# Kernel tuning notes

Measured on AMD Instinct MI355X. Metric: run time of the kernel, lower is better.

The kernel has to match this reference:

```python
import jax, jax.numpy as jnp
import numpy as np

B, N, C = 4, 20480, 128
H, HD = 8, 16           # num_heads, head_dim (C // H)
L = 4                   # number of WindowBasedGraphAttentionBlocks
NW, WS = 320, 64        # num_windows, window_size (N // NW)
SCALE = HD ** -0.5
EPS = 1e-5


def layernorm(x, g, b):
    mu = jnp.mean(x, axis=-1, keepdims=True)
    var = jnp.mean(jnp.square(x - mu), axis=-1, keepdims=True)
    return (x - mu) * jax.lax.rsqrt(var + EPS) * g + b


def setup_inputs() -> dict:
    key = jax.random.key(0)
    ks = jax.random.split(key, 8)
    x = jax.random.normal(ks[0], (B, N, C), dtype=jnp.float32)
    # geodesic window mapping: each of NW windows has exactly WS members, permuted
    window_ids = jnp.asarray(
        np.random.RandomState(0).permutation(np.repeat(np.arange(NW), WS)),
        dtype=jnp.int32)
    s = 0.02
    inp = {
        'x': x,
        'g1': jnp.ones((L, C), jnp.float32),
        'be1': jnp.zeros((L, C), jnp.float32),
        'Wqkv': jax.random.normal(ks[1], (L, C, 3 * C), jnp.float32) * s,
        'bqkv': jnp.zeros((L, 3 * C), jnp.float32),
        'rel_bias': jax.random.normal(ks[2], (L, H, 1, 1), jnp.float32) * s,
        'Wproj': jax.random.normal(ks[3], (L, C, C), jnp.float32) * s,
        'bproj': jnp.zeros((L, C), jnp.float32),
        'g2': jnp.ones((L, C), jnp.float32),
        'be2': jnp.zeros((L, C), jnp.float32),
        'W1': jax.random.normal(ks[4], (L, C, 4 * C), jnp.float32) * s,
        'b1': jnp.zeros((L, 4 * C), jnp.float32),
        'W2': jax.random.normal(ks[5], (L, 4 * C, C), jnp.float32) * s,
        'b2': jnp.zeros((L, C), jnp.float32),
        'window_ids': window_ids,
    }
    return inp


def _encoder(x, g1, be1, Wqkv, bqkv, rel_bias, Wproj, bproj, g2, be2,
             W1, b1, W2, b2, sort_idx, inv_idx):
    def step(x, p):
        (g1, be1, Wqkv, bqkv, rb, Wp, bp, g2, be2, W1, b1, W2, b2) = p
        shortcut = x
        # GeodesicWindowPartition: gather by argsort(window_ids), split into windows
        win = x[:, sort_idx, :].reshape(B * NW, WS, C)
        h = layernorm(win, g1, be1)
        qkv = (h @ Wqkv + bqkv).reshape(B * NW, WS, 3, H, HD)
        q = qkv[:, :, 0].transpose(0, 2, 1, 3)  # [BW, H, WS, HD]
        k = qkv[:, :, 1].transpose(0, 2, 1, 3)
        v = qkv[:, :, 2].transpose(0, 2, 1, 3)
        attn = jnp.einsum('whqd,whkd->whqk', q, k) * SCALE
        attn = attn + rb[None]                  # relative geometry bias [H,1,1]
        attn = jax.nn.softmax(attn, axis=-1)
        out = jnp.einsum('whqk,whkd->whqd', attn, v)
        out = out.transpose(0, 2, 1, 3).reshape(B * NW, WS, C)
        out = out @ Wp + bp                     # AttentionOutputProjection
        rec = out.reshape(B, N, C)[:, inv_idx, :]  # partition.reverse
        x = shortcut + rec
        h2 = layernorm(x, g2, be2)
        x = x + (jax.nn.gelu(h2 @ W1 + b1) @ W2 + b2)
        return x, None

    params = (g1, be1, Wqkv, bqkv, rel_bias, Wproj, bproj, g2, be2, W1, b1, W2, b2)
    x, _ = jax.lax.scan(step, x, params)
    return x


def reference(x, g1, be1, Wqkv, bqkv, rel_bias, Wproj, bproj, g2, be2,
              W1, b1, W2, b2, window_ids):
    sort_idx = jnp.argsort(window_ids)
    inv_idx = jnp.argsort(sort_idx)
    return _encoder(x, g1, be1, Wqkv, bqkv, rel_bias, Wproj, bproj, g2, be2,
                    W1, b1, W2, b2, sort_idx, inv_idx)
```

## Files before the change

### kernel.cpp

```cpp
#include <hip/hip_runtime.h>
#include <hip/hip_bf16.h>
#include <math.h>

#define Nn 20480
#define Cc 128
#define Hh 8
#define Ll 4
#define NWw 320
#define BN 81920

typedef short sv8 __attribute__((ext_vector_type(8)));
typedef __bf16 bfv8 __attribute__((ext_vector_type(8)));
typedef float f32x4 __attribute__((ext_vector_type(4)));

__device__ __forceinline__ f32x4 mfma16(sv8 a, sv8 b, f32x4 c) {
    return __builtin_amdgcn_mfma_f32_16x16x32_bf16(
        __builtin_bit_cast(bfv8, a), __builtin_bit_cast(bfv8, b), c, 0, 0, 0);
}
__device__ __forceinline__ ushort f2bf(float f) {
    uint u = __float_as_uint(f);
    u += 0x7fffu + ((u >> 16) & 1u);
    return (ushort)(u >> 16);
}
__device__ __forceinline__ uint pk2bf(float lo, float hi) {
    uint r;
    asm("v_cvt_pk_bf16_f32 %0, %1, %2" : "=v"(r) : "v"(lo), "v"(hi));
    return r;
}
__device__ __forceinline__ float fast_gelu(float x) {
    float z = 0.7978845608f * (x + 0.044715f * x * x * x);
    return x * __builtin_amdgcn_rcpf(1.0f + __expf(-2.0f * z));
}

__global__ __launch_bounds__(64) void rank_kernel(const int* __restrict__ wid,
        int* __restrict__ lrank, int* __restrict__ hist) {
    __shared__ int keys[64];
    int c = blockIdx.x, lane = threadIdx.x;
    for (int j = lane; j < NWw; j += 64) hist[c * NWw + j] = 0;
    int i = c * 64 + lane;
    int w = wid[i];
    keys[lane] = w;
    __syncthreads();
    int rank = 0, total = 0;
    for (int j = 0; j < 64; ++j) {
        int kj = keys[j];
        total += (kj == w);
        rank += (j < lane && kj == w) ? 1 : 0;
    }
    lrank[i] = rank;
    if (rank == 0) hist[c * NWw + w] = total;
}
__global__ __launch_bounds__(64) void prefix_kernel(int* __restrict__ hist) {
    int w = blockIdx.x, lane = threadIdx.x;
    int running = 0;
    for (int it = 0; it < NWw / 64; ++it) {
        int c = it * 64 + lane;
        int v = hist[c * NWw + w];
        int orig = v;
        #pragma unroll
        for (int d = 1; d < 64; d <<= 1) {
            int tt = __shfl_up(v, d, 64);
            if (lane >= d) v += tt;
        }
        hist[c * NWw + w] = running + v - orig;
        running += __shfl(v, 63, 64);
    }
}
__global__ __launch_bounds__(64) void scatter_kernel(const int* __restrict__ wid,
        const int* __restrict__ lrank, const int* __restrict__ hist,
        int* __restrict__ sidx) {
    int c = blockIdx.x, lane = threadIdx.x;
    int i = c * 64 + lane;
    int w = wid[i];
    sidx[w * 64 + hist[c * NWw + w] + lrank[i]] = i;
}

__global__ __launch_bounds__(256) void wconv_kernel(
    const float* __restrict__ Wqkv, const float* __restrict__ Wproj,
    const float* __restrict__ W1, const float* __restrict__ W2,
    ushort* __restrict__ wt) {
    int id = blockIdx.x * 256 + threadIdx.x;
    int l = id / 196608;
    int r = id % 196608;
    const float* src; int dst;
    if (r < 49152) { int n = r % 384, k = r / 384;
        src = Wqkv + l * 49152 + k * 384 + n; dst = l * 196608 + n * 128 + k; }
    else if (r < 65536) { int rr = r - 49152; int n = rr % 128, k = rr / 128;
        src = Wproj + l * 16384 + k * 128 + n; dst = l * 196608 + 49152 + n * 128 + k; }
    else if (r < 131072) { int rr = r - 65536; int n = rr % 512, k = rr / 512;
        src = W1 + l * 65536 + k * 512 + n; dst = l * 196608 + 65536 + n * 128 + k; }
    else { int rr = r - 131072; int n = rr % 128, k = rr / 128;
        src = W2 + l * 65536 + k * 128 + n; dst = l * 196608 + 131072 + n * 512 + k; }
    wt[dst] = f2bf(*src);
}

__global__ __launch_bounds__(256, 2) void attn_fused_kernel(
    const float* __restrict__ xsrc, float* __restrict__ xdst,
    const ushort* __restrict__ wqkvT, const float* __restrict__ bqkv,
    const float* __restrict__ relb, const ushort* __restrict__ wprojT,
    const float* __restrict__ bproj, const float* __restrict__ g1,
    const float* __restrict__ be1, const int* __restrict__ sidx) {
    __shared__ __align__(16) ushort hl_[64][128];
    __shared__ __align__(16) ushort qkn[64][256];
    __shared__ __align__(16) ushort vT[128][76];
    __shared__ __align__(16) ushort pt[4][16][76];
    __shared__ int ridx[64];

    int t = threadIdx.x;
    int wave = t >> 6, lane = t & 63;
    int lr = lane & 15, lg = lane >> 4;
    int wb = blockIdx.x;
    int bN = (wb / NWw) * Nn;
    int p0 = (wb % NWw) * 64;

    if (t < 64) ridx[t] = sidx[p0 + t];
    __syncthreads();

    {
        int hl2 = lane & 31, hb = lane >> 5;
        float4 gg = *(const float4*)(g1 + hl2 * 4);
        float4 bb = *(const float4*)(be1 + hl2 * 4);
        #pragma unroll
        for (int it = 0; it < 8; ++it) {
            int row = it * 8 + wave * 2 + hb;
            int gi = bN + ridx[row];
            float4 v = *(const float4*)(xsrc + (size_t)gi * Cc + hl2 * 4);
            float s = v.x + v.y + v.z + v.w;
            s += __shfl_xor(s, 1, 64);  s += __shfl_xor(s, 2, 64);
            s += __shfl_xor(s, 4, 64);  s += __shfl_xor(s, 8, 64);
            s += __shfl_xor(s, 16, 64);
            float mu = s * 0.0078125f;
            float d0 = v.x - mu, d1 = v.y - mu, d2 = v.z - mu, d3 = v.w - mu;
            float q = d0 * d0 + d1 * d1 + d2 * d2 + d3 * d3;
            q += __shfl_xor(q, 1, 64);  q += __shfl_xor(q, 2, 64);
            q += __shfl_xor(q, 4, 64);  q += __shfl_xor(q, 8, 64);
            q += __shfl_xor(q, 16, 64);
            float rs = rsqrtf(q * 0.0078125f + 1e-5f);
            uint2 pk;
            pk.x = pk2bf(d0 * rs * gg.x + bb.x, d1 * rs * gg.y + bb.y);
            pk.y = pk2bf(d2 * rs * gg.z + bb.z, d3 * rs * gg.w + bb.w);
            *(uint2*)&hl_[row][(hl2 * 4) ^ ((row & 7) << 3)] = pk;
        }
    }
    __syncthreads();

    {
        f32x4 acc[4][6] = {};
        #pragma unroll
        for (int ks = 0; ks < 4; ++ks) {
            int k0 = ks * 32 + lg * 8;
            sv8 a[4], b[6];
            #pragma unroll
            for (int rf = 0; rf < 4; ++rf) {
                int row = rf * 16 + lr;
                a[rf] = *(const sv8*)&hl_[row][k0 ^ ((row & 7) << 3)];
            }
            #pragma unroll
            for (int nf = 0; nf < 6; ++nf) {
                int gcol = (nf < 2 ? 32 * wave + nf * 16
                          : nf < 4 ? 128 + 32 * wave + (nf - 2) * 16
                                   : 256 + 32 * wave + (nf - 4) * 16) + lr;
                b[nf] = *(const sv8*)(wqkvT + (size_t)gcol * 128 + k0);
            }
            #pragma unroll
            for (int rf = 0; rf < 4; ++rf)
                #pragma unroll
                for (int nf = 0; nf < 6; ++nf)
                    acc[rf][nf] = mfma16(a[rf], b[nf], acc[rf][nf]);
        }
        #pragma unroll
        for (int nf = 0; nf < 6; ++nf) {
            int gcol = (nf < 2 ? 32 * wave + nf * 16
                      : nf < 4 ? 128 + 32 * wave + (nf - 2) * 16
                               : 256 + 32 * wave + (nf - 4) * 16) + lr;
            float bs = bqkv[gcol];
            if (nf < 4) {
                #pragma unroll
                for (int rf = 0; rf < 4; ++rf)
                    #pragma unroll
                    for (int r = 0; r < 4; ++r) {
                        int row = rf * 16 + lg * 4 + r;
                        qkn[row][gcol ^ ((row & 7) << 3)] = f2bf(acc[rf][nf][r] + bs);
                    }
            } else {
                int dcol = gcol - 256;
                #pragma unroll
                for (int rf = 0; rf < 4; ++rf) {
                    uint2 pk;
                    pk.x = pk2bf(acc[rf][nf][0] + bs, acc[rf][nf][1] + bs);
                    pk.y = pk2bf(acc[rf][nf][2] + bs, acc[rf][nf][3] + bs);
                    *(uint2*)&vT[dcol][rf * 16 + lg * 4] = pk;
                }
            }
        }
    }
    __syncthreads();

    f32x4 zz = {0.f, 0.f, 0.f, 0.f};
    #pragma unroll
    for (int hi = 0; hi < 2; ++hi) {
        int hh = wave * 2 + hi;
        float rb = relb[hh];
        sv8 bv[2];
        #pragma unroll
        for (int ks = 0; ks < 2; ++ks)
            bv[ks] = *(const sv8*)&vT[hh * 16 + lr][ks * 32 + lg * 8];
        sv8 aq[4], bk[4];
        sv8 z = {0, 0, 0, 0, 0, 0, 0, 0};
        bool lo = (lg < 2);
        #pragma unroll
        for (int f = 0; f < 4; ++f) {
            aq[f] = z; bk[f] = z;
            if (lo) {
                int row = f * 16 + lr;
                aq[f] = *(const sv8*)&qkn[row][(hh * 16 + lg * 8) ^ ((row & 7) << 3)];
                bk[f] = *(const sv8*)&qkn[row][(128 + hh * 16 + lg * 8) ^ ((row & 7) << 3)];
            }
        }
        f32x4 s[4][4];
        #pragma unroll
        for (int kt = 0; kt < 4; ++kt)
            #pragma unroll
            for (int qt = 0; qt < 4; ++qt)
                s[kt][qt] = mfma16(bk[kt], aq[qt], zz);

        f32x4 o[4];
        #pragma unroll
        for (int qt = 0; qt < 4; ++qt) {
            float v[16];
            #pragma unroll
            for (int kt = 0; kt < 4; ++kt)
                #pragma unroll
                for (int r = 0; r < 4; ++r)
                    v[kt * 4 + r] = s[kt][qt][r] * 0.25f + rb;
            float m0 = fmaxf(fmaxf(fmaxf(v[0], v[1]), fmaxf(v[2], v[3])),
                             fmaxf(fmaxf(v[4], v[5]), fmaxf(v[6], v[7])));
            float m1 = fmaxf(fmaxf(fmaxf(v[8], v[9]), fmaxf(v[10], v[11])),
                             fmaxf(fmaxf(v[12], v[13]), fmaxf(v[14], v[15])));
            float mx = fmaxf(m0, m1);
            mx = fmaxf(mx, __shfl_xor(mx, 16, 64));
            mx = fmaxf(mx, __shfl_xor(mx, 32, 64));
            float sum = 0.f;
            #pragma unroll
            for (int i = 0; i < 16; ++i) {
                v[i] = __expf(v[i] - mx);
                sum += v[i];
            }
            sum += __shfl_xor(sum, 16, 64);
            sum += __shfl_xor(sum, 32, 64);
            float inv = __builtin_amdgcn_rcpf(sum);
            #pragma unroll
            for (int kt = 0; kt < 4; ++kt) {
                uint2 pk;
                pk.x = pk2bf(v[kt * 4 + 0] * inv, v[kt * 4 + 1] * inv);
                pk.y = pk2bf(v[kt * 4 + 2] * inv, v[kt * 4 + 3] * inv);
                *(uint2*)&pt[wave][lr][kt * 16 + lg * 4] = pk;
            }
            sv8 ap0 = *(const sv8*)&pt[wave][lr][lg * 8];
            sv8 ap1 = *(const sv8*)&pt[wave][lr][32 + lg * 8];
            o[qt] = mfma16(ap0, bv[0], zz);
            o[qt] = mfma16(ap1, bv[1], o[qt]);
        }
        #pragma unroll
        for (int qt = 0; qt < 4; ++qt)
            #pragma unroll
            for (int r = 0; r < 4; ++r) {
                int row = qt * 16 + lg * 4 + r;
                hl_[row][(hh * 16 + lr) ^ ((row & 7) << 3)] = f2bf(o[qt][r]);
            }
    }
    __syncthreads();

    {
        f32x4 acc[4][2] = {};
        #pragma unroll
        for (int ks = 0; ks < 4; ++ks) {
            int k0 = ks * 32 + lg * 8;
            sv8 a[4], b[2];
            #pragma unroll
            for (int rf = 0; rf < 4; ++rf) {
                int row = rf * 16 + lr;
                a[rf] = *(const sv8*)&hl_[row][k0 ^ ((row & 7) << 3)];
            }
            #pragma unroll
            for (int nf = 0; nf < 2; ++nf)
                b[nf] = *(const sv8*)(wprojT + (size_t)(wave * 32 + nf * 16 + lr) * 128 + k0);
            #pragma unroll
            for (int rf = 0; rf < 4; ++rf)
                #pragma unroll
                for (int nf = 0; nf < 2; ++nf)
                    acc[rf][nf] = mfma16(a[rf], b[nf], acc[rf][nf]);
        }
        #pragma unroll
        for (int nf = 0; nf < 2; ++nf) {
            int col = wave * 32 + nf * 16 + lr;
            float bs = bproj[col];
            #pragma unroll
            for (int rf = 0; rf < 4; ++rf)
                #pragma unroll
                for (int r = 0; r < 4; ++r) {
                    int row = rf * 16 + lg * 4 + r;
                    int gi = bN + ridx[row];
                    size_t ad = (size_t)gi * Cc + col;
                    xdst[ad] = xsrc[ad] + acc[rf][nf][r] + bs;
                }
        }
    }
}

__global__ __launch_bounds__(256, 3) void mlp_fused_kernel(
    const float* __restrict__ xsrc, float* __restrict__ xdst,
    const ushort* __restrict__ w1T, const float* __restrict__ b1,
    const ushort* __restrict__ w2T, const float* __restrict__ b2,
    const float* __restrict__ g2, const float* __restrict__ be2) {
    __shared__ __align__(16) char smem[49152];
    ushort (*hl_)[128] = (ushort (*)[128])smem;
    ushort (*hid)[64][128] = (ushort (*)[64][128])(smem + 16384);
    int t = threadIdx.x, wave = t >> 6, lane = t & 63;
    int lr = lane & 15, lg = lane >> 4;
    int r0 = blockIdx.x * 64;

    {
        int hl2 = lane & 31, hb = lane >> 5;
        float4 gg = *(const float4*)(g2 + hl2 * 4);
        float4 bb = *(const float4*)(be2 + hl2 * 4);
        #pragma unroll
        for (int it = 0; it < 8; ++it) {
            int row = it * 8 + wave * 2 + hb;
            float4 v = *(const float4*)(xsrc + (size_t)(r0 + row) * Cc + hl2 * 4);
            float s = v.x + v.y + v.z + v.w;
            s += __shfl_xor(s, 1, 64);  s += __shfl_xor(s, 2, 64);
            s += __shfl_xor(s, 4, 64);  s += __shfl_xor(s, 8, 64);
            s += __shfl_xor(s, 16, 64);
            float mu = s * 0.0078125f;
            float d0 = v.x - mu, d1 = v.y - mu, d2 = v.z - mu, d3 = v.w - mu;
            float q = d0 * d0 + d1 * d1 + d2 * d2 + d3 * d3;
            q += __shfl_xor(q, 1, 64);  q += __shfl_xor(q, 2, 64);
            q += __shfl_xor(q, 4, 64);  q += __shfl_xor(q, 8, 64);
            q += __shfl_xor(q, 16, 64);
            float rs = rsqrtf(q * 0.0078125f + 1e-5f);
            uint2 pk;
            pk.x = pk2bf(d0 * rs * gg.x + bb.x, d1 * rs * gg.y + bb.y);
            pk.y = pk2bf(d2 * rs * gg.z + bb.z, d3 * rs * gg.w + bb.w);
            *(uint2*)&hl_[row][(hl2 * 4) ^ ((row & 7) << 3)] = pk;
        }
    }
    __syncthreads();

    f32x4 acc2[4][2] = {};
    #pragma unroll
    for (int c = 0; c < 4; ++c) {
        int cb = c & 1;
        f32x4 acc[4][2] = {};
        #pragma unroll
        for (int ks = 0; ks < 4; ++ks) {
            int k0 = ks * 32 + lg * 8;
            sv8 a[4], b[2];
            #pragma unroll
            for (int rf = 0; rf < 4; ++rf) {
                int row = rf * 16 + lr;
                a[rf] = *(const sv8*)&hl_[row][k0 ^ ((row & 7) << 3)];
            }
            #pragma unroll
            for (int nf = 0; nf < 2; ++nf)
                b[nf] = *(const sv8*)(w1T + (size_t)(c * 128 + wave * 32 + nf * 16 + lr) * 128 + k0);
            #pragma unroll
            for (int rf = 0; rf < 4; ++rf)
                #pragma unroll
                for (int nf = 0; nf < 2; ++nf)
                    acc[rf][nf] = mfma16(a[rf], b[nf], acc[rf][nf]);
        }
        #pragma unroll
        for (int nf = 0; nf < 2; ++nf) {
            int lcol = wave * 32 + nf * 16 + lr;
            float bs = b1[c * 128 + lcol];
            #pragma unroll
            for (int rf = 0; rf < 4; ++rf)
                #pragma unroll
                for (int r = 0; r < 4; ++r) {
                    int row = rf * 16 + lg * 4 + r;
                    hid[cb][row][lcol ^ ((row & 7) << 3)] = f2bf(fast_gelu(acc[rf][nf][r] + bs));
                }
        }
        __syncthreads();
        #pragma unroll
        for (int ks = 0; ks < 4; ++ks) {
            int k0 = ks * 32 + lg * 8;
            sv8 a[4], b[2];
            #pragma unroll
            for (int rf = 0; rf < 4; ++rf) {
                int row = rf * 16 + lr;
                a[rf] = *(const sv8*)&hid[cb][row][k0 ^ ((row & 7) << 3)];
            }
            #pragma unroll
            for (int nf = 0; nf < 2; ++nf)
                b[nf] = *(const sv8*)(w2T + (size_t)(wave * 32 + nf * 16 + lr) * 512 + c * 128 + k0);
            #pragma unroll
            for (int rf = 0; rf < 4; ++rf)
                #pragma unroll
                for (int nf = 0; nf < 2; ++nf)
                    acc2[rf][nf] = mfma16(a[rf], b[nf], acc2[rf][nf]);
        }
    }
    __syncthreads();

    {
        float* fh = (float*)smem;
        #pragma unroll
        for (int nf = 0; nf < 2; ++nf) {
            int col = wave * 32 + nf * 16 + lr;
            float bs = b2[col];
            #pragma unroll
            for (int rf = 0; rf < 4; ++rf)
                #pragma unroll
                for (int r = 0; r < 4; ++r) {
                    int row = rf * 16 + lg * 4 + r;
                    fh[row * 132 + col] = acc2[rf][nf][r] + bs;
                }
        }
        __syncthreads();
        #pragma unroll
        for (int j = 0; j < 8; ++j) {
            int idx = t + j * 256;
            int row = idx >> 5, c4 = (idx & 31) * 4;
            size_t ad = (size_t)(r0 + row) * Cc + c4;
            float4 xv = *(const float4*)(xsrc + ad);
            float4 hv = *(const float4*)&fh[row * 132 + c4];
            float4 ov = {xv.x + hv.x, xv.y + hv.y, xv.z + hv.z, xv.w + hv.w};
            *(float4*)(xdst + ad) = ov;
        }
    }
}

extern "C" void kernel_launch(void* const* d_in, const int* in_sizes, int n_in,
                              void* d_out, int out_size, void* d_ws, size_t ws_size,
                              hipStream_t stream) {
    const float* x_in   = (const float*)d_in[0];
    const float* g1     = (const float*)d_in[1];
    const float* be1    = (const float*)d_in[2];
    const float* Wqkv   = (const float*)d_in[3];
    const float* bqkv   = (const float*)d_in[4];
    const float* relb   = (const float*)d_in[5];
    const float* Wproj  = (const float*)d_in[6];
    const float* bproj  = (const float*)d_in[7];
    const float* g2     = (const float*)d_in[8];
    const float* be2    = (const float*)d_in[9];
    const float* W1     = (const float*)d_in[10];
    const float* b1     = (const float*)d_in[11];
    const float* W2     = (const float*)d_in[12];
    const float* b2     = (const float*)d_in[13];
    const int*   wid    = (const int*)d_in[14];

    size_t off = 0;
    float* x_ws = (float*)d_ws;                      off += (size_t)BN * Cc * 4;
    ushort* wt  = (ushort*)((char*)d_ws + off);      off += (size_t)786432 * 2;
    int* sidx   = (int*)((char*)d_ws + off);         off += (size_t)Nn * 4;
    int* lrank  = (int*)((char*)d_ws + off);         off += (size_t)Nn * 4;
    int* hist   = (int*)((char*)d_ws + off);         off += (size_t)NWw * NWw * 4;
    if (ws_size < off) return;

    rank_kernel<<<Nn / 64, 64, 0, stream>>>(wid, lrank, hist);
    prefix_kernel<<<NWw, 64, 0, stream>>>(hist);
    scatter_kernel<<<Nn / 64, 64, 0, stream>>>(wid, lrank, hist, sidx);
    wconv_kernel<<<786432 / 256, 256, 0, stream>>>(Wqkv, Wproj, W1, W2, wt);

    for (int l = 0; l < Ll; ++l) {
        const ushort* wqkvT  = wt + (size_t)l * 196608;
        const ushort* wprojT = wqkvT + 49152;
        const ushort* w1T    = wqkvT + 65536;
        const ushort* w2T    = wqkvT + 131072;
        const float* xsrc = (l == 0) ? x_in : x_ws;

        attn_fused_kernel<<<BN / 64, 256, 0, stream>>>(
            xsrc, x_ws, wqkvT, bqkv + l * 384, relb + l * Hh,
            wprojT, bproj + l * Cc, g1 + l * Cc, be1 + l * Cc, sidx);

        float* xdst = (l == Ll - 1) ? (float*)d_out : x_ws;
        mlp_fused_kernel<<<BN / 64, 256, 0, stream>>>(
            x_ws, xdst, w1T, b1 + l * 512, w2T, b2 + l * Cc,
            g2 + l * Cc, be2 + l * Cc);
    }
}
```

Measured before the change: 474.7 us.

## Shrink MLP tile to 32 rows with two waves and transposed first GEMM

The fused MLP kernel now processes 32 rows per block with 128 threads (two waves), each wave covering 64 hidden/output columns instead of 32. The first GEMM is computed transposed (weights as the A operand), so each lane holds four consecutive hidden columns and can write GELU outputs as packed 8-byte stores with vectorized bias loads. Shared memory halves, which may let more blocks fit per CU and doubles the grid size. The cost is that weight fragments are re-read from global memory by twice as many blocks, and per-wave accumulator use grows.

```diff
diff --git a/kernel.cpp b/kernel.cpp
--- a/kernel.cpp
+++ b/kernel.cpp
@@ -308,17 +308,17 @@
     }
 }
 
-__global__ __launch_bounds__(256, 3) void mlp_fused_kernel(
+__global__ __launch_bounds__(128, 3) void mlp_fused_kernel(
     const float* __restrict__ xsrc, float* __restrict__ xdst,
     const ushort* __restrict__ w1T, const float* __restrict__ b1,
     const ushort* __restrict__ w2T, const float* __restrict__ b2,
     const float* __restrict__ g2, const float* __restrict__ be2) {
-    __shared__ __align__(16) char smem[49152];
+    __shared__ __align__(16) char smem[24576];
     ushort (*hl_)[128] = (ushort (*)[128])smem;
-    ushort (*hid)[64][128] = (ushort (*)[64][128])(smem + 16384);
+    ushort (*hid)[32][128] = (ushort (*)[32][128])(smem + 8192);
     int t = threadIdx.x, wave = t >> 6, lane = t & 63;
     int lr = lane & 15, lg = lane >> 4;
-    int r0 = blockIdx.x * 64;
+    int r0 = blockIdx.x * 32;
 
     {
         int hl2 = lane & 31, hb = lane >> 5;
@@ -326,7 +326,7 @@
         float4 bb = *(const float4*)(be2 + hl2 * 4);
         #pragma unroll
         for (int it = 0; it < 8; ++it) {
-            int row = it * 8 + wave * 2 + hb;
+            int row = it * 4 + wave * 2 + hb;
             float4 v = *(const float4*)(xsrc + (size_t)(r0 + row) * Cc + hl2 * 4);
             float s = v.x + v.y + v.z + v.w;
             s += __shfl_xor(s, 1, 64);  s += __shfl_xor(s, 2, 64);
@@ -347,59 +347,64 @@
     }
     __syncthreads();
 
-    f32x4 acc2[4][2] = {};
+    f32x4 acc2[2][4] = {};
     #pragma unroll
     for (int c = 0; c < 4; ++c) {
         int cb = c & 1;
-        f32x4 acc[4][2] = {};
+        f32x4 acc_s[4][2] = {};
         #pragma unroll
         for (int ks = 0; ks < 4; ++ks) {
             int k0 = ks * 32 + lg * 8;
-            sv8 a[4], b[2];
-            #pragma unroll
-            for (int rf = 0; rf < 4; ++rf) {
-                int row = rf * 16 + lr;
-                a[rf] = *(const sv8*)&hl_[row][k0 ^ ((row & 7) << 3)];
-            }
-            #pragma unroll
-            for (int nf = 0; nf < 2; ++nf)
-                b[nf] = *(const sv8*)(w1T + (size_t)(c * 128 + wave * 32 + nf * 16 + lr) * 128 + k0);
-            #pragma unroll
-            for (int rf = 0; rf < 4; ++rf)
-                #pragma unroll
-                for (int nf = 0; nf < 2; ++nf)
-                    acc[rf][nf] = mfma16(a[rf], b[nf], acc[rf][nf]);
-        }
-        #pragma unroll
-        for (int nf = 0; nf < 2; ++nf) {
-            int lcol = wave * 32 + nf * 16 + lr;
-            float bs = b1[c * 128 + lcol];
-            #pragma unroll
-            for (int rf = 0; rf < 4; ++rf)
-                #pragma unroll
-                for (int r = 0; r < 4; ++r) {
-                    int row = rf * 16 + lg * 4 + r;
-                    hid[cb][row][lcol ^ ((row & 7) << 3)] = f2bf(fast_gelu(acc[rf][nf][r] + bs));
-                }
+            sv8 hfr[2], wfr[4];
+            #pragma unroll
+            for (int tf = 0; tf < 2; ++tf) {
+                int row = tf * 16 + lr;
+                hfr[tf] = *(const sv8*)&hl_[row][k0 ^ ((row & 7) << 3)];
+            }
+            #pragma unroll
+            for (int hf = 0; hf < 4; ++hf)
+                wfr[hf] = *(const sv8*)(w1T + (size_t)(c * 128 + wave * 64 + hf * 16 + lr) * 128 + k0);
+            #pragma unroll
+            for (int hf = 0; hf < 4; ++hf)
+                #pragma unroll
+                for (int tf = 0; tf < 2; ++tf)
+                    acc_s[hf][tf] = mfma16(wfr[hf], hfr[tf], acc_s[hf][tf]);
+        }
+        #pragma unroll
+        for (int hf = 0; hf < 4; ++hf) {
+            int hcol = wave * 64 + hf * 16 + lg * 4;
+            float4 bs4 = *(const float4*)(b1 + c * 128 + hcol);
+            #pragma unroll
+            for (int tf = 0; tf < 2; ++tf) {
+                int row = tf * 16 + lr;
+                float g0 = fast_gelu(acc_s[hf][tf][0] + bs4.x);
+                float g1v = fast_gelu(acc_s[hf][tf][1] + bs4.y);
+                float g2v = fast_gelu(acc_s[hf][tf][2] + bs4.z);
+                float g3 = fast_gelu(acc_s[hf][tf][3] + bs4.w);
+                uint2 pk;
+                pk.x = pk2bf(g0, g1v);
+                pk.y = pk2bf(g2v, g3);
+                *(uint2*)&hid[cb][row][hcol ^ ((row & 7) << 3)] = pk;
+            }
         }
         __syncthreads();
         #pragma unroll
         for (int ks = 0; ks < 4; ++ks) {
             int k0 = ks * 32 + lg * 8;
-            sv8 a[4], b[2];
-            #pragma unroll
-            for (int rf = 0; rf < 4; ++rf) {
-                int row = rf * 16 + lr;
-                a[rf] = *(const sv8*)&hid[cb][row][k0 ^ ((row & 7) << 3)];
-            }
-            #pragma unroll
-            for (int nf = 0; nf < 2; ++nf)
-                b[nf] = *(const sv8*)(w2T + (size_t)(wave * 32 + nf * 16 + lr) * 512 + c * 128 + k0);
-            #pragma unroll
-            for (int rf = 0; rf < 4; ++rf)
-                #pragma unroll
-                for (int nf = 0; nf < 2; ++nf)
-                    acc2[rf][nf] = mfma16(a[rf], b[nf], acc2[rf][nf]);
+            sv8 a[2], b[4];
+            #pragma unroll
+            for (int tf = 0; tf < 2; ++tf) {
+                int row = tf * 16 + lr;
+                a[tf] = *(const sv8*)&hid[cb][row][k0 ^ ((row & 7) << 3)];
+            }
+            #pragma unroll
+            for (int nf = 0; nf < 4; ++nf)
+                b[nf] = *(const sv8*)(w2T + (size_t)(wave * 64 + nf * 16 + lr) * 512 + c * 128 + k0);
+            #pragma unroll
+            for (int tf = 0; tf < 2; ++tf)
+                #pragma unroll
+                for (int nf = 0; nf < 4; ++nf)
+                    acc2[tf][nf] = mfma16(a[tf], b[nf], acc2[tf][nf]);
         }
     }
     __syncthreads();
@@ -407,21 +412,21 @@
     {
         float* fh = (float*)smem;
         #pragma unroll
-        for (int nf = 0; nf < 2; ++nf) {
-            int col = wave * 32 + nf * 16 + lr;
+        for (int nf = 0; nf < 4; ++nf) {
+            int col = wave * 64 + nf * 16 + lr;
             float bs = b2[col];
             #pragma unroll
-            for (int rf = 0; rf < 4; ++rf)
+            for (int tf = 0; tf < 2; ++tf)
                 #pragma unroll
                 for (int r = 0; r < 4; ++r) {
-                    int row = rf * 16 + lg * 4 + r;
-                    fh[row * 132 + col] = acc2[rf][nf][r] + bs;
+                    int row = tf * 16 + lg * 4 + r;
+                    fh[row * 132 + col] = acc2[tf][nf][r] + bs;
                 }
         }
         __syncthreads();
         #pragma unroll
         for (int j = 0; j < 8; ++j) {
-            int idx = t + j * 256;
+            int idx = t + j * 128;
             int row = idx >> 5, c4 = (idx & 31) * 4;
             size_t ad = (size_t)(r0 + row) * Cc + c4;
             float4 xv = *(const float4*)(xsrc + ad);
@@ -476,7 +481,7 @@
             wprojT, bproj + l * Cc, g1 + l * Cc, be1 + l * Cc, sidx);
 
         float* xdst = (l == Ll - 1) ? (float*)d_out : x_ws;
-        mlp_fused_kernel<<<BN / 64, 256, 0, stream>>>(
+        mlp_fused_kernel<<<BN / 32, 128, 0, stream>>>(
             x_ws, xdst, w1T, b1 + l * 512, w2T, b2 + l * Cc,
             g2 + l * Cc, be2 + l * Cc);
     }
```

Result: slower. 611.8 us (+28.9%).
